# Optimization experiments

Measured on AMD Instinct MI355X. Metric: run time of the kernel, lower is better.

## Reference

```python
import jax, jax.numpy as jnp
import numpy as np

N_NODES = 100000
D = 256            # in_channels
H = 256            # hidden_channels
E = 1000000        # number of query pairs


def setup_inputs() -> dict:
    key = jax.random.key(0)
    ks = jax.random.split(key, 8)
    x = jax.random.normal(ks[0], (N_NODES, D), dtype=jnp.float32)
    edge_index = jax.random.randint(ks[1], (2, 1000), 0, N_NODES, dtype=jnp.int64)
    edge_pairs = jax.random.randint(ks[2], (E, 2), 0, N_NODES, dtype=jnp.int64)
    # MLP params (Linear stores y = x @ W + b, W shaped [in, out])
    s1 = 1.0 / np.sqrt(D)
    s2 = 1.0 / np.sqrt(H)
    s3 = 1.0 / np.sqrt(H // 2)
    W1 = jax.random.uniform(ks[3], (D, H), jnp.float32, -s1, s1)
    b1 = jnp.zeros((H,), jnp.float32)
    W2 = jax.random.uniform(ks[4], (H, H // 2), jnp.float32, -s2, s2)
    b2 = jnp.zeros((H // 2,), jnp.float32)
    W3 = jax.random.uniform(ks[5], (H // 2, 1), jnp.float32, -s3, s3)
    b3 = jnp.zeros((1,), jnp.float32)
    return {"x": x, "W1": W1, "b1": b1, "W2": W2, "b2": b2,
            "W3": W3, "b3": b3, "edge_index": edge_index, "edge_pairs": edge_pairs}


def reference(x, W1, b1, W2, b2, W3, b3, edge_index, edge_pairs):
    # Gather node pairs and form elementwise-product pair features [E, D]
    feats = x[edge_pairs[:, 0]] * x[edge_pairs[:, 1]]
    # 3-layer MLP (dropout inactive at inference)
    h = jax.nn.relu(feats @ W1 + b1)
    h = jax.nn.relu(h @ W2 + b2)
    scores = h @ W3 + b3
    return scores.reshape(-1)
```

## Files before the change

kernel.cpp:

```cpp
#include <hip/hip_runtime.h>


typedef __attribute__((ext_vector_type(8))) short short8;
typedef __attribute__((ext_vector_type(4))) float floatx4;
typedef __attribute__((ext_vector_type(4))) unsigned uintx4;
typedef __attribute__((ext_vector_type(2))) int intx2;

#define MT 64
#define NTHREADS 1024
#define NBLOCKS 256

__device__ __forceinline__ unsigned short f2bf(float f) {
  union { float f; unsigned u; } a; a.f = f;
  unsigned r = a.u + 0x7FFFu + ((a.u >> 16) & 1u);
  return (unsigned short)(r >> 16);
}

__device__ __forceinline__ unsigned pkbf(float lo, float hi) {
  unsigned r;
  asm("v_cvt_pk_bf16_f32 %0, %1, %2" : "=v"(r) : "v"(lo), "v"(hi));
  return r;
}

__device__ __forceinline__ unsigned bfmul2(unsigned ua, unsigned ub) {
  float lo = __uint_as_float(ua << 16)          * __uint_as_float(ub << 16);
  float hi = __uint_as_float(ua & 0xFFFF0000u) * __uint_as_float(ub & 0xFFFF0000u);
  return pkbf(lo, hi);
}

__global__ void prep_kernel(const float* __restrict__ x,
                            const float* __restrict__ W1,
                            const float* __restrict__ W2,
                            unsigned short* __restrict__ xb,
                            unsigned short* __restrict__ w1t,
                            unsigned short* __restrict__ w2t, int n4) {
  int i = blockIdx.x * blockDim.x + threadIdx.x;
  if (i < n4) {
    float4 v = ((const float4*)x)[i];
    ushort4 o;
    o.x = f2bf(v.x); o.y = f2bf(v.y); o.z = f2bf(v.z); o.w = f2bf(v.w);
    ((ushort4*)xb)[i] = o;
  } else {
    int j = i - n4;
    if (j < 256 * 256) {
      int k = j >> 8, n = j & 255;
      w1t[n * 256 + k] = f2bf(W1[k * 256 + n]);
    } else {
      j -= 256 * 256;
      if (j < 128 * 256) {
        int k = j >> 7, n = j & 127;
        w2t[n * 256 + k] = f2bf(W2[k * 128 + n]);
      }
    }
  }
}

__global__ __launch_bounds__(NTHREADS, 4) void mlp_kernel(
    const unsigned short* __restrict__ xb,
    const unsigned short* __restrict__ w1t,
    const unsigned short* __restrict__ w2t,
    const float* __restrict__ b1,
    const float* __restrict__ b2,
    const float* __restrict__ w3,
    const float* __restrict__ b3,
    const int* __restrict__ ep,
    float* __restrict__ out,
    int E)
{
  __shared__ __align__(16) unsigned short feats[2][MT * 256];
  __shared__ __align__(16) unsigned short h1buf[MT * 256];
  __shared__ float part[MT][9];

  const int tid  = threadIdx.x;
  const int wv   = tid >> 6;
  const int lane = tid & 63;
  const int q    = lane >> 4;
  const int r16  = lane & 15;
  const int c    = tid & 31;
  const int mr0  = tid >> 5;

  const int ntiles = (E + MT - 1) / MT;

  const int n1  = wv * 16 + r16;
  const int mg2 = wv >> 3;
  const int ng2 = wv & 7;
  const int n2  = ng2 * 16 + r16;

  short8 bv1[8], bv2[8];
  {
    const unsigned short* const b1p = w1t + n1 * 256 + q * 8;
    const unsigned short* const b2p = w2t + n2 * 256 + q * 8;
    #pragma unroll
    for (int kt = 0; kt < 8; ++kt) {
      bv1[kt] = *(const short8*)(b1p + kt * 32);
      bv2[kt] = *(const short8*)(b2p + kt * 32);
    }
  }
  const float bias1 = b1[n1];
  const float bias2 = b2[n2];
  const float w3v   = w3[n2];
  const float b3v   = b3[0];

  intx2 uv0, uv1;
  {
    const int t0 = blockIdx.x;
    #pragma unroll
    for (int s = 0; s < 2; ++s) {
      int m = mr0 + 32 * s;
      int g = t0 * MT + m; if (g >= E) g = E - 1;
      intx2 uv = __builtin_nontemporal_load((const intx2*)(ep + 2 * (size_t)g));
      uintx4 a = *(const uintx4*)(xb + ((size_t)(unsigned)uv.x << 8) + (c << 3));
      uintx4 b = *(const uintx4*)(xb + ((size_t)(unsigned)uv.y << 8) + (c << 3));
      uintx4 pv;
      #pragma unroll
      for (int tt = 0; tt < 4; ++tt) pv[tt] = bfmul2(a[tt], b[tt]);
      *(uintx4*)((char*)feats[0] + m * 512 + ((c ^ (m & 15)) << 4)) = pv;
    }
    int t1 = t0 + NBLOCKS;
    int g0 = t1 * MT + mr0;      if (g0 >= E) g0 = E - 1;
    int g1 = t1 * MT + mr0 + 32; if (g1 >= E) g1 = E - 1;
    uv0 = __builtin_nontemporal_load((const intx2*)(ep + 2 * (size_t)g0));
    uv1 = __builtin_nontemporal_load((const intx2*)(ep + 2 * (size_t)g1));
  }
  __syncthreads();

  int fp = 0;
  for (int t = blockIdx.x; t < ntiles; t += NBLOCKS) {
    uintx4 ra0 = *(const uintx4*)(xb + ((size_t)(unsigned)uv0.x << 8) + (c << 3));
    uintx4 rb0 = *(const uintx4*)(xb + ((size_t)(unsigned)uv0.y << 8) + (c << 3));
    uintx4 ra1 = *(const uintx4*)(xb + ((size_t)(unsigned)uv1.x << 8) + (c << 3));
    uintx4 rb1 = *(const uintx4*)(xb + ((size_t)(unsigned)uv1.y << 8) + (c << 3));

    intx2 nv0, nv1;
    {
      int t2 = t + 2 * NBLOCKS;
      int g0 = t2 * MT + mr0;      if (g0 >= E) g0 = E - 1;
      int g1 = t2 * MT + mr0 + 32; if (g1 >= E) g1 = E - 1;
      nv0 = __builtin_nontemporal_load((const intx2*)(ep + 2 * (size_t)g0));
      nv1 = __builtin_nontemporal_load((const intx2*)(ep + 2 * (size_t)g1));
    }

    floatx4 acc[4];
    #pragma unroll
    for (int i = 0; i < 4; ++i) acc[i] = (floatx4){0.f, 0.f, 0.f, 0.f};

    const char* const a1base = (const char*)feats[fp] + r16 * 512;
    #pragma unroll
    for (int kt = 0; kt < 8; ++kt) {
      const int aoff = (kt << 6) ^ ((q ^ r16) << 4);
      short8 av[4];
      #pragma unroll
      for (int mt = 0; mt < 4; ++mt)
        av[mt] = *(const short8*)(a1base + mt * (16 * 512) + aoff);
      #pragma unroll
      for (int mt = 0; mt < 4; ++mt)
        acc[mt] = __builtin_amdgcn_mfma_f32_16x16x32_bf16(av[mt], bv1[kt], acc[mt], 0, 0, 0);
    }

    {
      char* const hb = (char*)h1buf;
      const int chb = n1 >> 3;
      const int eo  = (n1 & 7) << 1;
      #pragma unroll
      for (int mt = 0; mt < 4; ++mt) {
        #pragma unroll
        for (int rp = 0; rp < 2; ++rp) {
          float h0 = fmaxf(acc[mt][2 * rp]     + bias1, 0.f);
          float h1 = fmaxf(acc[mt][2 * rp + 1] + bias1, 0.f);
          unsigned pk = pkbf(h0, h1);
          int m0 = mt * 16 + q * 4 + 2 * rp;
          *(unsigned short*)(hb + m0 * 512 + ((chb ^ (m0 & 15)) << 4) + eo) =
              (unsigned short)pk;
          *(unsigned short*)(hb + (m0 + 1) * 512 + ((chb ^ ((m0 + 1) & 15)) << 4) + eo) =
              (unsigned short)(pk >> 16);
        }
      }
    }
    __syncthreads();

    {
      char* const bufn = (char*)feats[fp ^ 1];
      uintx4 pv0, pv1;
      #pragma unroll
      for (int tt = 0; tt < 4; ++tt) pv0[tt] = bfmul2(ra0[tt], rb0[tt]);
      #pragma unroll
      for (int tt = 0; tt < 4; ++tt) pv1[tt] = bfmul2(ra1[tt], rb1[tt]);
      const int m0 = mr0, m1 = mr0 + 32;
      *(uintx4*)(bufn + m0 * 512 + ((c ^ (m0 & 15)) << 4)) = pv0;
      *(uintx4*)(bufn + m1 * 512 + ((c ^ (m1 & 15)) << 4)) = pv1;
    }

    floatx4 acc2[2];
    acc2[0] = (floatx4){0.f, 0.f, 0.f, 0.f};
    acc2[1] = (floatx4){0.f, 0.f, 0.f, 0.f};
    const char* const a2base = (const char*)h1buf + (mg2 * 32 + r16) * 512;
    #pragma unroll
    for (int kt = 0; kt < 8; ++kt) {
      const int aoff = (kt << 6) ^ ((q ^ r16) << 4);
      short8 av0 = *(const short8*)(a2base + aoff);
      short8 av1 = *(const short8*)(a2base + 16 * 512 + aoff);
      acc2[0] = __builtin_amdgcn_mfma_f32_16x16x32_bf16(av0, bv2[kt], acc2[0], 0, 0, 0);
      acc2[1] = __builtin_amdgcn_mfma_f32_16x16x32_bf16(av1, bv2[kt], acc2[1], 0, 0, 0);
    }

    {
      #pragma unroll
      for (int mt = 0; mt < 2; ++mt) {
        #pragma unroll
        for (int r = 0; r < 4; ++r) {
          float h = fmaxf(acc2[mt][r] + bias2, 0.f);
          float pp = h * w3v;
          pp += __shfl_xor(pp, 1);
          pp += __shfl_xor(pp, 2);
          pp += __shfl_xor(pp, 4);
          pp += __shfl_xor(pp, 8);
          if (r16 == 0)
            part[mg2 * 32 + mt * 16 + q * 4 + r][ng2] = pp;
        }
      }
    }
    __syncthreads();

    if (tid < MT) {
      int g = t * MT + tid;
      if (g < E) {
        float s = (part[tid][0] + part[tid][1]) + (part[tid][2] + part[tid][3]) +
                  (part[tid][4] + part[tid][5]) + (part[tid][6] + part[tid][7]);
        out[g] = s + b3v;
      }
    }

    fp ^= 1;
    uv0 = nv0; uv1 = nv1;
  }
}

extern "C" void kernel_launch(void* const* d_in, const int* in_sizes, int n_in,
                              void* d_out, int out_size, void* d_ws, size_t ws_size,
                              hipStream_t stream) {
  const float* x  = (const float*)d_in[0];
  const float* W1 = (const float*)d_in[1];
  const float* b1 = (const float*)d_in[2];
  const float* W2 = (const float*)d_in[3];
  const float* b2 = (const float*)d_in[4];
  const float* W3 = (const float*)d_in[5];
  const float* b3 = (const float*)d_in[6];
  const int*   ep = (const int*)d_in[8];
  float* out = (float*)d_out;

  const int NX = in_sizes[0];
  const int E  = in_sizes[8] / 2;

  unsigned short* xb  = (unsigned short*)d_ws;
  unsigned short* w1t = (unsigned short*)((char*)d_ws + (size_t)NX * 2);
  unsigned short* w2t = w1t + 256 * 256;

  const int n4 = NX / 4;
  const int prep_threads = n4 + 256 * 256 + 128 * 256;
  prep_kernel<<<(prep_threads + 255) / 256, 256, 0, stream>>>(x, W1, W2, xb, w1t, w2t, n4);
  mlp_kernel<<<NBLOCKS, NTHREADS, 0, stream>>>(xb, w1t, w2t, b1, b2, W3, b3, ep, out, E);
}
```

Before: 451.8 us.

## Warp-specialize layer-1 and layer-2 waves with cross-tile software pipelining

Splits the 16 waves into two groups: eight producer waves compute layer 1 for the current tile, each covering 32 output columns. Eight consumer waves compute layer 2 plus the W3 reduction for the previous tile, using a double-buffered h1 buffer and a double-buffered partial-sum array. This cuts the per-tile barriers from two to one and lets the two layers overlap. The cost is more LDS, a pipeline prologue and epilogue, and uneven per-wave MFMA work. The final out write also drops the g<E bound check, which assumes E is a multiple of the tile size.

```diff
diff --git a/kernel.cpp b/kernel.cpp
--- a/kernel.cpp
+++ b/kernel.cpp
@@ -9,6 +9,9 @@
 #define MT 64
 #define NTHREADS 1024
 #define NBLOCKS 256
+
+#define KEEP8(a) asm volatile("" : "+v"(a[0]), "+v"(a[1]), "+v"(a[2]), "+v"(a[3]), \
+                                   "+v"(a[4]), "+v"(a[5]), "+v"(a[6]), "+v"(a[7]))
 
 __device__ __forceinline__ unsigned short f2bf(float f) {
   union { float f; unsigned u; } a; a.f = f;
@@ -68,8 +71,8 @@
     int E)
 {
   __shared__ __align__(16) unsigned short feats[2][MT * 256];
-  __shared__ __align__(16) unsigned short h1buf[MT * 256];
-  __shared__ float part[MT][9];
+  __shared__ __align__(16) unsigned short h1b[2][MT * 256];
+  __shared__ __align__(16) float part[2][MT][4];
 
   const int tid  = threadIdx.x;
   const int wv   = tid >> 6;
@@ -78,45 +81,53 @@
   const int r16  = lane & 15;
   const int c    = tid & 31;
   const int mr0  = tid >> 5;
+  const bool isP = (wv < 8);
 
   const int ntiles = (E + MT - 1) / MT;
-
-  const int n1  = wv * 16 + r16;
-  const int mg2 = wv >> 3;
-  const int ng2 = wv & 7;
-  const int n2  = ng2 * 16 + r16;
-
-  short8 bv1[8], bv2[8];
-  {
-    const unsigned short* const b1p = w1t + n1 * 256 + q * 8;
-    const unsigned short* const b2p = w2t + n2 * 256 + q * 8;
+  const int b = blockIdx.x;
+  const int nloc = (ntiles - 1 - b) / NBLOCKS + 1;
+
+  short8 wA[2][8];
+  float bA[2], wS[2];
+  if (isP) {
     #pragma unroll
-    for (int kt = 0; kt < 8; ++kt) {
-      bv1[kt] = *(const short8*)(b1p + kt * 32);
-      bv2[kt] = *(const short8*)(b2p + kt * 32);
-    }
-  }
-  const float bias1 = b1[n1];
-  const float bias2 = b2[n2];
-  const float w3v   = w3[n2];
-  const float b3v   = b3[0];
+    for (int ct = 0; ct < 2; ++ct) {
+      const int n = wv * 32 + ct * 16 + r16;
+      const unsigned short* p = w1t + n * 256 + q * 8;
+      #pragma unroll
+      for (int kt = 0; kt < 8; ++kt) wA[ct][kt] = *(const short8*)(p + kt * 32);
+      bA[ct] = b1[n];
+      wS[ct] = 0.f;
+    }
+  } else {
+    const int cg = (wv - 8) & 3;
+    #pragma unroll
+    for (int ct = 0; ct < 2; ++ct) {
+      const int n = cg * 32 + ct * 16 + r16;
+      const unsigned short* p = w2t + n * 256 + q * 8;
+      #pragma unroll
+      for (int kt = 0; kt < 8; ++kt) wA[ct][kt] = *(const short8*)(p + kt * 32);
+      bA[ct] = b2[n];
+      wS[ct] = w3[n];
+    }
+  }
+  const float b3v = b3[0];
 
   intx2 uv0, uv1;
   {
-    const int t0 = blockIdx.x;
     #pragma unroll
     for (int s = 0; s < 2; ++s) {
       int m = mr0 + 32 * s;
-      int g = t0 * MT + m; if (g >= E) g = E - 1;
+      int g = b * MT + m; if (g >= E) g = E - 1;
       intx2 uv = __builtin_nontemporal_load((const intx2*)(ep + 2 * (size_t)g));
       uintx4 a = *(const uintx4*)(xb + ((size_t)(unsigned)uv.x << 8) + (c << 3));
-      uintx4 b = *(const uintx4*)(xb + ((size_t)(unsigned)uv.y << 8) + (c << 3));
+      uintx4 bv = *(const uintx4*)(xb + ((size_t)(unsigned)uv.y << 8) + (c << 3));
       uintx4 pv;
       #pragma unroll
-      for (int tt = 0; tt < 4; ++tt) pv[tt] = bfmul2(a[tt], b[tt]);
+      for (int tt = 0; tt < 4; ++tt) pv[tt] = bfmul2(a[tt], bv[tt]);
       *(uintx4*)((char*)feats[0] + m * 512 + ((c ^ (m & 15)) << 4)) = pv;
     }
-    int t1 = t0 + NBLOCKS;
+    const int t1 = b + NBLOCKS;
     int g0 = t1 * MT + mr0;      if (g0 >= E) g0 = E - 1;
     int g1 = t1 * MT + mr0 + 32; if (g1 >= E) g1 = E - 1;
     uv0 = __builtin_nontemporal_load((const intx2*)(ep + 2 * (size_t)g0));
@@ -124,61 +135,103 @@
   }
   __syncthreads();
 
-  int fp = 0;
-  for (int t = blockIdx.x; t < ntiles; t += NBLOCKS) {
-    uintx4 ra0 = *(const uintx4*)(xb + ((size_t)(unsigned)uv0.x << 8) + (c << 3));
-    uintx4 rb0 = *(const uintx4*)(xb + ((size_t)(unsigned)uv0.y << 8) + (c << 3));
-    uintx4 ra1 = *(const uintx4*)(xb + ((size_t)(unsigned)uv1.x << 8) + (c << 3));
-    uintx4 rb1 = *(const uintx4*)(xb + ((size_t)(unsigned)uv1.y << 8) + (c << 3));
-
-    intx2 nv0, nv1;
-    {
-      int t2 = t + 2 * NBLOCKS;
-      int g0 = t2 * MT + mr0;      if (g0 >= E) g0 = E - 1;
-      int g1 = t2 * MT + mr0 + 32; if (g1 >= E) g1 = E - 1;
-      nv0 = __builtin_nontemporal_load((const intx2*)(ep + 2 * (size_t)g0));
-      nv1 = __builtin_nontemporal_load((const intx2*)(ep + 2 * (size_t)g1));
-    }
-
-    floatx4 acc[4];
-    #pragma unroll
-    for (int i = 0; i < 4; ++i) acc[i] = (floatx4){0.f, 0.f, 0.f, 0.f};
-
-    const char* const a1base = (const char*)feats[fp] + r16 * 512;
-    #pragma unroll
-    for (int kt = 0; kt < 8; ++kt) {
-      const int aoff = (kt << 6) ^ ((q ^ r16) << 4);
-      short8 av[4];
-      #pragma unroll
-      for (int mt = 0; mt < 4; ++mt)
-        av[mt] = *(const short8*)(a1base + mt * (16 * 512) + aoff);
-      #pragma unroll
-      for (int mt = 0; mt < 4; ++mt)
-        acc[mt] = __builtin_amdgcn_mfma_f32_16x16x32_bf16(av[mt], bv1[kt], acc[mt], 0, 0, 0);
-    }
-
-    {
-      char* const hb = (char*)h1buf;
-      const int chb = n1 >> 3;
-      const int eo  = (n1 & 7) << 1;
-      #pragma unroll
-      for (int mt = 0; mt < 4; ++mt) {
-        #pragma unroll
-        for (int rp = 0; rp < 2; ++rp) {
-          float h0 = fmaxf(acc[mt][2 * rp]     + bias1, 0.f);
-          float h1 = fmaxf(acc[mt][2 * rp + 1] + bias1, 0.f);
-          unsigned pk = pkbf(h0, h1);
-          int m0 = mt * 16 + q * 4 + 2 * rp;
-          *(unsigned short*)(hb + m0 * 512 + ((chb ^ (m0 & 15)) << 4) + eo) =
-              (unsigned short)pk;
-          *(unsigned short*)(hb + (m0 + 1) * 512 + ((chb ^ ((m0 + 1) & 15)) << 4) + eo) =
-              (unsigned short)(pk >> 16);
-        }
-      }
-    }
-    __syncthreads();
-
-    {
+  for (int i = 0; i <= nloc; ++i) {
+    const int fp = i & 1;
+    const bool stg = (i + 1 < nloc);
+
+    uintx4 ra0, rb0, ra1, rb1;
+    if (stg) {
+      ra0 = *(const uintx4*)(xb + ((size_t)(unsigned)uv0.x << 8) + (c << 3));
+      rb0 = *(const uintx4*)(xb + ((size_t)(unsigned)uv0.y << 8) + (c << 3));
+      ra1 = *(const uintx4*)(xb + ((size_t)(unsigned)uv1.x << 8) + (c << 3));
+      rb1 = *(const uintx4*)(xb + ((size_t)(unsigned)uv1.y << 8) + (c << 3));
+    }
+
+    if (isP) {
+      KEEP8(wA[0]); KEEP8(wA[1]);
+      if (i < nloc) {
+        floatx4 acc[4][2];
+        #pragma unroll
+        for (int mt = 0; mt < 4; ++mt) {
+          acc[mt][0] = (floatx4){0.f, 0.f, 0.f, 0.f};
+          acc[mt][1] = (floatx4){0.f, 0.f, 0.f, 0.f};
+        }
+        const char* const a1base = (const char*)feats[fp] + r16 * 512;
+        #pragma unroll
+        for (int kt = 0; kt < 8; ++kt) {
+          const int aoff = (kt << 6) ^ ((q ^ r16) << 4);
+          #pragma unroll
+          for (int mt = 0; mt < 4; ++mt) {
+            short8 av = *(const short8*)(a1base + mt * (16 * 512) + aoff);
+            acc[mt][0] = __builtin_amdgcn_mfma_f32_16x16x32_bf16(av, wA[0][kt], acc[mt][0], 0, 0, 0);
+            acc[mt][1] = __builtin_amdgcn_mfma_f32_16x16x32_bf16(av, wA[1][kt], acc[mt][1], 0, 0, 0);
+          }
+        }
+        char* const hb = (char*)h1b[fp];
+        #pragma unroll
+        for (int ct = 0; ct < 2; ++ct) {
+          const int n1  = wv * 32 + ct * 16 + r16;
+          const int chb = n1 >> 3;
+          const int eo  = (n1 & 7) << 1;
+          #pragma unroll
+          for (int mt = 0; mt < 4; ++mt) {
+            #pragma unroll
+            for (int rp = 0; rp < 2; ++rp) {
+              float h0 = fmaxf(acc[mt][ct][2 * rp]     + bA[ct], 0.f);
+              float h1 = fmaxf(acc[mt][ct][2 * rp + 1] + bA[ct], 0.f);
+              unsigned pk = pkbf(h0, h1);
+              int m0 = mt * 16 + q * 4 + 2 * rp;
+              *(unsigned short*)(hb + m0 * 512 + ((chb ^ (m0 & 15)) << 4) + eo) =
+                  (unsigned short)pk;
+              *(unsigned short*)(hb + (m0 + 1) * 512 + ((chb ^ ((m0 + 1) & 15)) << 4) + eo) =
+                  (unsigned short)(pk >> 16);
+            }
+          }
+        }
+      }
+      if (tid < MT && i >= 2) {
+        floatx4 pr = *(const floatx4*)part[fp ^ 1][tid];
+        out[(b + (i - 2) * NBLOCKS) * MT + tid] =
+            (pr[0] + pr[1]) + (pr[2] + pr[3]) + b3v;
+      }
+    } else {
+      KEEP8(wA[0]); KEEP8(wA[1]);
+      if (i >= 1) {
+        const int cw = wv - 8, mg = cw >> 2, cg = cw & 3;
+        floatx4 acc2[2][2];
+        acc2[0][0] = (floatx4){0.f, 0.f, 0.f, 0.f};
+        acc2[0][1] = (floatx4){0.f, 0.f, 0.f, 0.f};
+        acc2[1][0] = (floatx4){0.f, 0.f, 0.f, 0.f};
+        acc2[1][1] = (floatx4){0.f, 0.f, 0.f, 0.f};
+        const char* const a2base = (const char*)h1b[fp ^ 1] + (mg * 32 + r16) * 512;
+        #pragma unroll
+        for (int kt = 0; kt < 8; ++kt) {
+          const int aoff = (kt << 6) ^ ((q ^ r16) << 4);
+          short8 av0 = *(const short8*)(a2base + aoff);
+          short8 av1 = *(const short8*)(a2base + 16 * 512 + aoff);
+          acc2[0][0] = __builtin_amdgcn_mfma_f32_16x16x32_bf16(av0, wA[0][kt], acc2[0][0], 0, 0, 0);
+          acc2[0][1] = __builtin_amdgcn_mfma_f32_16x16x32_bf16(av0, wA[1][kt], acc2[0][1], 0, 0, 0);
+          acc2[1][0] = __builtin_amdgcn_mfma_f32_16x16x32_bf16(av1, wA[0][kt], acc2[1][0], 0, 0, 0);
+          acc2[1][1] = __builtin_amdgcn_mfma_f32_16x16x32_bf16(av1, wA[1][kt], acc2[1][1], 0, 0, 0);
+        }
+        #pragma unroll
+        for (int mt = 0; mt < 2; ++mt) {
+          #pragma unroll
+          for (int r = 0; r < 4; ++r) {
+            float pp = fmaxf(acc2[mt][0][r] + bA[0], 0.f) * wS[0]
+                     + fmaxf(acc2[mt][1][r] + bA[1], 0.f) * wS[1];
+            pp += __shfl_xor(pp, 1);
+            pp += __shfl_xor(pp, 2);
+            pp += __shfl_xor(pp, 4);
+            pp += __shfl_xor(pp, 8);
+            if (r16 == 0)
+              part[fp][mg * 32 + mt * 16 + q * 4 + r][cg] = pp;
+          }
+        }
+      }
+    }
+
+    if (stg) {
       char* const bufn = (char*)feats[fp ^ 1];
       uintx4 pv0, pv1;
       #pragma unroll
@@ -188,50 +241,20 @@
       const int m0 = mr0, m1 = mr0 + 32;
       *(uintx4*)(bufn + m0 * 512 + ((c ^ (m0 & 15)) << 4)) = pv0;
       *(uintx4*)(bufn + m1 * 512 + ((c ^ (m1 & 15)) << 4)) = pv1;
-    }
-
-    floatx4 acc2[2];
-    acc2[0] = (floatx4){0.f, 0.f, 0.f, 0.f};
-    acc2[1] = (floatx4){0.f, 0.f, 0.f, 0.f};
-    const char* const a2base = (const char*)h1buf + (mg2 * 32 + r16) * 512;
-    #pragma unroll
-    for (int kt = 0; kt < 8; ++kt) {
-      const int aoff = (kt << 6) ^ ((q ^ r16) << 4);
-      short8 av0 = *(const short8*)(a2base + aoff);
-      short8 av1 = *(const short8*)(a2base + 16 * 512 + aoff);
-      acc2[0] = __builtin_amdgcn_mfma_f32_16x16x32_bf16(av0, bv2[kt], acc2[0], 0, 0, 0);
-      acc2[1] = __builtin_amdgcn_mfma_f32_16x16x32_bf16(av1, bv2[kt], acc2[1], 0, 0, 0);
-    }
-
-    {
-      #pragma unroll
-      for (int mt = 0; mt < 2; ++mt) {
-        #pragma unroll
-        for (int r = 0; r < 4; ++r) {
-          float h = fmaxf(acc2[mt][r] + bias2, 0.f);
-          float pp = h * w3v;
-          pp += __shfl_xor(pp, 1);
-          pp += __shfl_xor(pp, 2);
-          pp += __shfl_xor(pp, 4);
-          pp += __shfl_xor(pp, 8);
-          if (r16 == 0)
-            part[mg2 * 32 + mt * 16 + q * 4 + r][ng2] = pp;
-        }
-      }
+
+      const int t2 = b + (i + 2) * NBLOCKS;
+      int g0 = t2 * MT + mr0;      if (g0 >= E) g0 = E - 1;
+      int g1 = t2 * MT + mr0 + 32; if (g1 >= E) g1 = E - 1;
+      uv0 = __builtin_nontemporal_load((const intx2*)(ep + 2 * (size_t)g0));
+      uv1 = __builtin_nontemporal_load((const intx2*)(ep + 2 * (size_t)g1));
     }
     __syncthreads();
-
-    if (tid < MT) {
-      int g = t * MT + tid;
-      if (g < E) {
-        float s = (part[tid][0] + part[tid][1]) + (part[tid][2] + part[tid][3]) +
-                  (part[tid][4] + part[tid][5]) + (part[tid][6] + part[tid][7]);
-        out[g] = s + b3v;
-      }
-    }
-
-    fp ^= 1;
-    uv0 = nv0; uv1 = nv1;
+  }
+
+  if (tid < MT) {
+    floatx4 pr = *(const floatx4*)part[nloc & 1][tid];
+    out[(b + (nloc - 1) * NBLOCKS) * MT + tid] =
+        (pr[0] + pr[1]) + (pr[2] + pr[3]) + b3v;
   }
 }
 
```

New measurement: 756.8 us. 67.5% more time.
